# Performance work log

Hardware: AMD Instinct MI355X
Metric: run time of the kernel (lower is better)

The kernel has to match this reference:

```python
import jax, jax.numpy as jnp
import numpy as np

THRESHOLD = 0.5
NEGPOS_RATIO = 3
VARIANCES = (0.1, 0.2)

B, P, C, T = 64, 24564, 81, 50


def point_form(boxes):
    # center form (cx,cy,w,h) -> corner form (x1,y1,x2,y2)
    return jnp.concatenate([boxes[:, :2] - boxes[:, 2:] / 2,
                            boxes[:, :2] + boxes[:, 2:] / 2], axis=-1)


def jaccard(box_a, box_b):
    # box_a [T,4], box_b [P,4], corner form -> IoU [T,P]
    max_xy = jnp.minimum(box_a[:, None, 2:], box_b[None, :, 2:])
    min_xy = jnp.maximum(box_a[:, None, :2], box_b[None, :, :2])
    inter = jnp.prod(jnp.clip(max_xy - min_xy, 0.0), axis=-1)
    area_a = jnp.prod(box_a[:, 2:] - box_a[:, :2], axis=-1)[:, None]
    area_b = jnp.prod(box_b[:, 2:] - box_b[:, :2], axis=-1)[None, :]
    return inter / (area_a + area_b - inter)


def encode(matched, priors, variances):
    # matched [P,4] corner form, priors [P,4] center form
    g_cxcy = (matched[:, :2] + matched[:, 2:]) / 2 - priors[:, :2]
    g_cxcy = g_cxcy / (variances[0] * priors[:, 2:])
    g_wh = (matched[:, 2:] - matched[:, :2]) / priors[:, 2:]
    g_wh = jnp.log(g_wh) / variances[1]
    return jnp.concatenate([g_cxcy, g_wh], axis=-1)


def match_one(truths, labels, priors):
    # truths [T,4] corner, labels [T] int, priors [P,4] center form
    overlaps = jaccard(truths, point_form(priors))          # [T,P]
    best_prior_idx = jnp.argmax(overlaps, axis=1)           # [T] best prior per gt
    best_truth_overlap = jnp.max(overlaps, axis=0)          # [P]
    best_truth_idx = jnp.argmax(overlaps, axis=0)           # [P]
    # ensure every gt keeps its best prior
    best_truth_overlap = best_truth_overlap.at[best_prior_idx].set(2.0)
    best_truth_idx = best_truth_idx.at[best_prior_idx].set(jnp.arange(truths.shape[0]))
    matched = truths[best_truth_idx]                        # [P,4]
    conf = labels[best_truth_idx] + 1                       # background = 0
    conf = jnp.where(best_truth_overlap < THRESHOLD, 0, conf)
    loc = encode(matched, priors, VARIANCES)                # [P,4]
    return loc, conf


def setup_inputs() -> dict:
    key = jax.random.key(0)
    k1, k2, k3, k4, k5, k6, k7 = jax.random.split(key, 7)
    loc_data = jax.random.normal(k1, (B, P, 4), jnp.float32)
    conf_data = jax.random.normal(k2, (B, P, C), jnp.float32)
    # priors: center form, in-bounds
    ctr = 0.05 + 0.9 * jax.random.uniform(k3, (P, 2))
    wh = 0.05 + 0.25 * jax.random.uniform(k4, (P, 2))
    priors = jnp.concatenate([ctr, wh], axis=-1).astype(jnp.float32)
    # gt boxes: corner form with x2>x1, y2>y1
    xy1 = 0.7 * jax.random.uniform(k5, (B, T, 2))
    gwh = 0.05 + 0.25 * jax.random.uniform(k6, (B, T, 2))
    targets_boxes = jnp.concatenate([xy1, jnp.minimum(xy1 + gwh, 1.0)], axis=-1).astype(jnp.float32)
    targets_labels = jax.random.randint(k7, (B, T), 0, C - 1, jnp.int32)
    return {"loc_data": loc_data, "conf_data": conf_data, "priors": priors,
            "targets_boxes": targets_boxes, "targets_labels": targets_labels}


def reference(loc_data, conf_data, priors, targets_boxes, targets_labels):
    num, num_priors, _ = loc_data.shape
    # per-image matching, batched with vmap
    loc_t, conf_t = jax.vmap(lambda t, l: match_one(t, l, priors))(targets_boxes, targets_labels)
    pos = conf_t > 0                                         # [B,P]
    # localization: smooth-L1 over positives, sum
    diff = loc_data - loc_t
    ad = jnp.abs(diff)
    sl1 = jnp.where(ad < 1.0, 0.5 * diff * diff, ad - 0.5)
    loss_l = jnp.sum(sl1 * pos[..., None])
    # confidence: cross entropy = logsumexp - gathered logit
    logsm = jax.nn.log_softmax(conf_data, axis=-1)
    ce = -jnp.take_along_axis(logsm, conf_t[..., None], axis=-1)[..., 0]  # [B,P]
    # hard negative mining: rank losses among negatives
    loss_mine = jnp.where(pos, 0.0, ce)
    num_pos = jnp.sum(pos, axis=1)                           # [B]
    num_neg = jnp.minimum(NEGPOS_RATIO * num_pos, num_priors - 1)
    idx_rank = jnp.argsort(jnp.argsort(-loss_mine, axis=1), axis=1)
    neg = idx_rank < num_neg[:, None]
    loss_c = jnp.sum(jnp.where(pos | neg, ce, 0.0))
    n = jnp.maximum(jnp.sum(num_pos), 1).astype(loc_data.dtype)
    return jnp.stack([loss_l / n, loss_c / n])
```

## Files before the change

kernel.cpp:

```cpp
#include <hip/hip_runtime.h>
#include <cstdint>
#include <cstddef>

#define NB 64
#define NP 24564
#define NC 81
#define NT 50
#define NROWS (NB*NP)
#define TCH 10
#define NSEG 8
#define SEGLEN ((NP + NSEG - 1)/NSEG)

__device__ __forceinline__ unsigned long long umax64(unsigned long long a, unsigned long long b){
  return a > b ? a : b;
}

__global__ __launch_bounds__(256) void k_match(
    const float* __restrict__ priors, const float* __restrict__ tboxes,
    float* __restrict__ bto, int* __restrict__ bti)
{
  __shared__ float tb[NT*4];
  __shared__ float ta[NT];
  const int tid = threadIdx.x;
  const int b = blockIdx.y;
  if (tid < NT*4) tb[tid] = tboxes[b*NT*4 + tid];
  __syncthreads();
  if (tid < NT) ta[tid] = (tb[tid*4+2]-tb[tid*4+0]) * (tb[tid*4+3]-tb[tid*4+1]);
  __syncthreads();
  const int p = blockIdx.x*256 + tid;
  if (p >= NP) return;
  const float4 pr = ((const float4* __restrict__)priors)[p];
  const float px1 = pr.x - 0.5f*pr.z, py1 = pr.y - 0.5f*pr.w;
  const float px2 = pr.x + 0.5f*pr.z, py2 = pr.y + 0.5f*pr.w;
  const float pa  = pr.z * pr.w;
  float best = -1.0f; int bidx = 0;
  for (int t = 0; t < NT; ++t){
    const float x1 = tb[t*4+0], y1 = tb[t*4+1], x2 = tb[t*4+2], y2 = tb[t*4+3];
    float ix = fminf(x2, px2) - fmaxf(x1, px1);
    float iy = fminf(y2, py2) - fmaxf(y1, py1);
    ix = fmaxf(ix, 0.0f); iy = fmaxf(iy, 0.0f);
    const float inter = ix * iy;
    const float iou = inter / (ta[t] + pa - inter);
    if (iou > best){ best = iou; bidx = t; }
  }
  bto[b*NP + p] = best;
  bti[b*NP + p] = bidx;
}

__global__ __launch_bounds__(256) void k_bestprior(
    const float* __restrict__ priors, const float* __restrict__ tboxes,
    unsigned long long* __restrict__ bpk)
{
  __shared__ float tb[TCH*4];
  __shared__ float ta[TCH];
  __shared__ unsigned long long red[256*TCH];
  const int tid = threadIdx.x;
  const int b  = blockIdx.x;
  const int t0 = blockIdx.y * TCH;
  const int i0 = blockIdx.z * SEGLEN;
  const int iend = min(i0 + SEGLEN, NP);
  if (tid < TCH*4) tb[tid] = tboxes[(b*NT + t0)*4 + tid];
  __syncthreads();
  if (tid < TCH) ta[tid] = (tb[tid*4+2]-tb[tid*4+0]) * (tb[tid*4+3]-tb[tid*4+1]);
  __syncthreads();

  unsigned long long best[TCH];
  #pragma unroll
  for (int j = 0; j < TCH; ++j) best[j] = 0ULL;

  for (int i = i0 + tid; i < iend; i += 256){
    const float4 pr = ((const float4* __restrict__)priors)[i];
    const float px1 = pr.x - 0.5f*pr.z, py1 = pr.y - 0.5f*pr.w;
    const float px2 = pr.x + 0.5f*pr.z, py2 = pr.y + 0.5f*pr.w;
    const float pa  = pr.z * pr.w;
    const unsigned long long low = (unsigned long long)(~(unsigned)i);
    #pragma unroll
    for (int j = 0; j < TCH; ++j){
      float ix = fminf(tb[j*4+2], px2) - fmaxf(tb[j*4+0], px1);
      float iy = fminf(tb[j*4+3], py2) - fmaxf(tb[j*4+1], py1);
      ix = fmaxf(ix, 0.0f); iy = fmaxf(iy, 0.0f);
      const float inter = ix * iy;
      const float iou = inter / (ta[j] + pa - inter);
      const unsigned long long key =
          ((unsigned long long)__float_as_uint(iou) << 32) | low;
      best[j] = umax64(best[j], key);
    }
  }
  #pragma unroll
  for (int j = 0; j < TCH; ++j) red[tid*TCH + j] = best[j];
  __syncthreads();
  for (int s = 128; s > 0; s >>= 1){
    if (tid < s){
      #pragma unroll
      for (int j = 0; j < TCH; ++j)
        red[tid*TCH + j] = umax64(red[tid*TCH + j], red[(tid+s)*TCH + j]);
    }
    __syncthreads();
  }
  if (tid < TCH)
    atomicMax(&bpk[b*NT + t0 + tid], red[tid]);
}

__global__ void k_force(const unsigned long long* __restrict__ bpk,
                        float* __restrict__ bto, int* __restrict__ bti)
{
  const int b = threadIdx.x;
  if (b >= NB) return;
  for (int t = 0; t < NT; ++t){
    const int p = (int)(~(unsigned)(bpk[b*NT + t] & 0xffffffffULL));
    bto[b*NP + p] = 2.0f;
    bti[b*NP + p] = t;
  }
}

__global__ __launch_bounds__(256) void k_ce(
    const float* __restrict__ conf, const float* __restrict__ loc,
    const float* __restrict__ priors, const float* __restrict__ tboxes,
    const int* __restrict__ tlabels,
    const float* __restrict__ bto, const int* __restrict__ bti,
    float* __restrict__ mine, float* __restrict__ ce_pos,
    float* __restrict__ loss_l, int* __restrict__ num_pos)
{
  const int tid = threadIdx.x;
  const int b = blockIdx.y;
  const int p0 = blockIdx.x*256 + tid;
  const bool active = p0 < NP;
  const int p = active ? p0 : (NP - 1);
  const int r = b*NP + p;
  const size_t e0 = (size_t)r * NC;
  const size_t a0 = e0 & ~(size_t)3;
  const int s = (int)(e0 & 3);

  const float4* __restrict__ c4 = (const float4* __restrict__)conf + (a0 >> 2);
  float4 w[21];
  #pragma unroll
  for (int j = 0; j < 21; ++j) w[j] = c4[j];

  const float ov = bto[r];
  const int   ti = bti[r];
  const int  cls = (ov < 0.5f) ? 0 : (tlabels[b*NT + ti] + 1);
  const float lg = conf[e0 + cls];

  const float NI = -INFINITY;
  w[0].x  = (s > 0) ? NI : w[0].x;
  w[0].y  = (s > 1) ? NI : w[0].y;
  w[0].z  = (s > 2) ? NI : w[0].z;
  w[20].y = (s < 1) ? NI : w[20].y;
  w[20].z = (s < 2) ? NI : w[20].z;
  w[20].w = (s < 3) ? NI : w[20].w;

  float m = w[0].w;
  #pragma unroll
  for (int j = 0; j < 21; ++j)
    m = fmaxf(m, fmaxf(fmaxf(w[j].x, w[j].y), fmaxf(w[j].z, w[j].w)));

  float a0s = 0.f, a1s = 0.f, a2s = 0.f, a3s = 0.f;
  #pragma unroll
  for (int j = 0; j < 21; ++j){
    a0s += __expf(w[j].x - m);
    a1s += __expf(w[j].y - m);
    a2s += __expf(w[j].z - m);
    a3s += __expf(w[j].w - m);
  }
  const float ce = m + __logf((a0s + a1s) + (a2s + a3s)) - lg;

  const bool pos = active && (cls > 0);
  if (active) mine[r] = pos ? 0.0f : ce;

  float cp = pos ? ce : 0.0f;
  float ll = 0.0f;
  int   pc = pos ? 1 : 0;
  if (pos){
    const float4 pr = ((const float4* __restrict__)priors)[p];
    const float4 t4 = ((const float4* __restrict__)tboxes)[b*NT + ti];
    const float gcx = ((t4.x + t4.z)*0.5f - pr.x) / (0.1f*pr.z);
    const float gcy = ((t4.y + t4.w)*0.5f - pr.y) / (0.1f*pr.w);
    const float gw  = __logf((t4.z - t4.x) / pr.z) * 5.0f;
    const float gh  = __logf((t4.w - t4.y) / pr.w) * 5.0f;
    const float4 ld = ((const float4* __restrict__)loc)[r];
    float d, ad;
    d = ld.x - gcx; ad = fabsf(d); ll += (ad < 1.0f) ? 0.5f*d*d : ad - 0.5f;
    d = ld.y - gcy; ad = fabsf(d); ll += (ad < 1.0f) ? 0.5f*d*d : ad - 0.5f;
    d = ld.z - gw;  ad = fabsf(d); ll += (ad < 1.0f) ? 0.5f*d*d : ad - 0.5f;
    d = ld.w - gh;  ad = fabsf(d); ll += (ad < 1.0f) ? 0.5f*d*d : ad - 0.5f;
  }

  #pragma unroll
  for (int off = 32; off > 0; off >>= 1){
    cp += __shfl_down(cp, off);
    ll += __shfl_down(ll, off);
    pc += __shfl_down(pc, off);
  }
  __shared__ float rcp[4], rll[4];
  __shared__ int rpc[4];
  const int wv = tid >> 6;
  if ((tid & 63) == 0){ rcp[wv] = cp; rll[wv] = ll; rpc[wv] = pc; }
  __syncthreads();
  if (tid == 0){
    atomicAdd(&ce_pos[b], (rcp[0]+rcp[1])+(rcp[2]+rcp[3]));
    atomicAdd(&loss_l[b], (rll[0]+rll[1])+(rll[2]+rll[3]));
    atomicAdd(&num_pos[b], (rpc[0]+rpc[1])+(rpc[2]+rpc[3]));
  }
}

__global__ __launch_bounds__(256) void k_topk(
    const float* __restrict__ mine, const int* __restrict__ num_pos,
    float* __restrict__ topk)
{
  const int b = blockIdx.x;
  const int tid = threadIdx.x;
  const float* __restrict__ d = mine + (size_t)b * NP;
  const int k = min(3 * num_pos[b], NP - 1);

  __shared__ unsigned hist[256];
  __shared__ unsigned sfx[257];
  __shared__ unsigned s_prefix;
  __shared__ int s_rem;
  __shared__ float s_sum;

  if (k <= 0){
    if (tid == 0) topk[b] = 0.0f;
    return;
  }
  if (tid == 0){ s_prefix = 0u; s_rem = k; s_sum = 0.0f; }
  __syncthreads();

  for (int pass = 0; pass < 4; ++pass){
    const int shift = 24 - pass*8;
    hist[tid] = 0u;
    __syncthreads();
    const unsigned pref = s_prefix;
    #pragma unroll 4
    for (int i = tid; i < NP; i += 256){
      const unsigned u = __float_as_uint(d[i]);
      const bool cand = (pass == 0) || ((u >> (shift + 8)) == pref);
      if (cand) atomicAdd(&hist[(u >> shift) & 255u], 1u);
    }
    __syncthreads();
    sfx[tid] = hist[tid];
    if (tid == 0) sfx[256] = 0u;
    __syncthreads();
    for (int off = 1; off < 256; off <<= 1){
      const unsigned add = (tid + off < 256) ? sfx[tid + off] : 0u;
      __syncthreads();
      sfx[tid] += add;
      __syncthreads();
    }
    const int rem = s_rem;
    __syncthreads();
    if ((int)sfx[tid] >= rem && (int)sfx[tid + 1] < rem){
      s_prefix = (pref << 8) | (unsigned)tid;
      s_rem = rem - (int)sfx[tid + 1];
    }
    __syncthreads();
  }

  const unsigned kb = s_prefix;
  const int rem = s_rem;
  const float kv = __uint_as_float(kb);
  float acc = 0.0f;
  #pragma unroll 4
  for (int i = tid; i < NP; i += 256){
    const float x = d[i];
    if (__float_as_uint(x) > kb) acc += x;
  }
  atomicAdd(&s_sum, acc);
  __syncthreads();
  if (tid == 0) topk[b] = s_sum + (float)rem * kv;
}

__global__ void k_final(const int* __restrict__ num_pos,
                        const float* __restrict__ loss_l,
                        const float* __restrict__ ce_pos,
                        const float* __restrict__ topk,
                        float* __restrict__ out)
{
  const int tid = threadIdx.x;
  int   np = num_pos[tid];
  float ll = loss_l[tid];
  float cp = ce_pos[tid];
  float tk = topk[tid];
  #pragma unroll
  for (int off = 32; off > 0; off >>= 1){
    np += __shfl_down(np, off);
    ll += __shfl_down(ll, off);
    cp += __shfl_down(cp, off);
    tk += __shfl_down(tk, off);
  }
  if (tid == 0){
    const float n = (float)max(np, 1);
    out[0] = ll / n;
    out[1] = (cp + tk) / n;
  }
}

extern "C" void kernel_launch(void* const* d_in, const int* in_sizes, int n_in,
                              void* d_out, int out_size, void* d_ws, size_t ws_size,
                              hipStream_t stream)
{
  const float* loc     = (const float*)d_in[0];
  const float* conf    = (const float*)d_in[1];
  const float* priors  = (const float*)d_in[2];
  const float* tboxes  = (const float*)d_in[3];
  const int*   tlabels = (const int*)d_in[4];
  float* out = (float*)d_out;

  char* ws = (char*)d_ws;
  int*   num_pos = (int*)(ws + 0);
  float* loss_l  = (float*)(ws + 256);
  float* ce_pos  = (float*)(ws + 512);
  float* topk    = (float*)(ws + 768);
  unsigned long long* bpk = (unsigned long long*)(ws + 1024);
  float* bto  = (float*)(ws + 26624);
  int*   bti  = (int*)  (ws + 26624 + 4*(size_t)NROWS);
  float* mine = (float*)(ws + 26624 + 8*(size_t)NROWS);

  hipMemsetAsync(ws, 0, 26624, stream);

  dim3 gA((NP + 255)/256, NB);
  k_match<<<gA, 256, 0, stream>>>(priors, tboxes, bto, bti);

  dim3 gA2(NB, NT/TCH, NSEG);
  k_bestprior<<<gA2, 256, 0, stream>>>(priors, tboxes, bpk);

  k_force<<<1, 64, 0, stream>>>(bpk, bto, bti);

  dim3 gC((NP + 255)/256, NB);
  k_ce<<<gC, 256, 0, stream>>>(conf, loc, priors, tboxes, tlabels,
                               bto, bti, mine, ce_pos, loss_l, num_pos);

  k_topk<<<NB, 256, 0, stream>>>(mine, num_pos, topk);

  k_final<<<1, 64, 0, stream>>>(num_pos, loss_l, ce_pos, topk, out);
}
```

Before: 880.5 us.

## Fuse IoU matching into CE kernel and widen top-k selection

Removes the separate per-prior matching kernel and the force kernel. Each CE thread now computes its best-truth IoU against shared-memory truth boxes and applies the forced best-prior overrides from the packed keys, which avoids writing and re-reading the per-row overlap and index arrays. The best-prior reduction switches to wave shuffles, and its segment count goes from 8 to 16. The top-k radix select moves to 1024 threads with float4 loads and a wave-level suffix scan. The trade-off is more ALU work and shared-memory traffic inside the bandwidth-bound CE kernel.

Result: faster. 781.5 us (-11.2%).

```diff
diff --git a/kernel.cpp b/kernel.cpp
--- a/kernel.cpp
+++ b/kernel.cpp
@@ -5,46 +5,14 @@
 #define NB 64
 #define NP 24564
 #define NC 81
+#define NROWS (NB*NP)
 #define NT 50
-#define NROWS (NB*NP)
 #define TCH 10
-#define NSEG 8
-#define SEGLEN ((NP + NSEG - 1)/NSEG)
+#define NSEG 16
+#define SEGLEN 1536
 
 __device__ __forceinline__ unsigned long long umax64(unsigned long long a, unsigned long long b){
   return a > b ? a : b;
-}
-
-__global__ __launch_bounds__(256) void k_match(
-    const float* __restrict__ priors, const float* __restrict__ tboxes,
-    float* __restrict__ bto, int* __restrict__ bti)
-{
-  __shared__ float tb[NT*4];
-  __shared__ float ta[NT];
-  const int tid = threadIdx.x;
-  const int b = blockIdx.y;
-  if (tid < NT*4) tb[tid] = tboxes[b*NT*4 + tid];
-  __syncthreads();
-  if (tid < NT) ta[tid] = (tb[tid*4+2]-tb[tid*4+0]) * (tb[tid*4+3]-tb[tid*4+1]);
-  __syncthreads();
-  const int p = blockIdx.x*256 + tid;
-  if (p >= NP) return;
-  const float4 pr = ((const float4* __restrict__)priors)[p];
-  const float px1 = pr.x - 0.5f*pr.z, py1 = pr.y - 0.5f*pr.w;
-  const float px2 = pr.x + 0.5f*pr.z, py2 = pr.y + 0.5f*pr.w;
-  const float pa  = pr.z * pr.w;
-  float best = -1.0f; int bidx = 0;
-  for (int t = 0; t < NT; ++t){
-    const float x1 = tb[t*4+0], y1 = tb[t*4+1], x2 = tb[t*4+2], y2 = tb[t*4+3];
-    float ix = fminf(x2, px2) - fmaxf(x1, px1);
-    float iy = fminf(y2, py2) - fmaxf(y1, py1);
-    ix = fmaxf(ix, 0.0f); iy = fmaxf(iy, 0.0f);
-    const float inter = ix * iy;
-    const float iou = inter / (ta[t] + pa - inter);
-    if (iou > best){ best = iou; bidx = t; }
-  }
-  bto[b*NP + p] = best;
-  bti[b*NP + p] = bidx;
 }
 
 __global__ __launch_bounds__(256) void k_bestprior(
@@ -53,7 +21,7 @@
 {
   __shared__ float tb[TCH*4];
   __shared__ float ta[TCH];
-  __shared__ unsigned long long red[256*TCH];
+  __shared__ unsigned long long part[4][TCH];
   const int tid = threadIdx.x;
   const int b  = blockIdx.x;
   const int t0 = blockIdx.y * TCH;
@@ -87,29 +55,22 @@
     }
   }
   #pragma unroll
-  for (int j = 0; j < TCH; ++j) red[tid*TCH + j] = best[j];
-  __syncthreads();
-  for (int s = 128; s > 0; s >>= 1){
-    if (tid < s){
-      #pragma unroll
-      for (int j = 0; j < TCH; ++j)
-        red[tid*TCH + j] = umax64(red[tid*TCH + j], red[(tid+s)*TCH + j]);
-    }
-    __syncthreads();
-  }
-  if (tid < TCH)
-    atomicMax(&bpk[b*NT + t0 + tid], red[tid]);
-}
-
-__global__ void k_force(const unsigned long long* __restrict__ bpk,
-                        float* __restrict__ bto, int* __restrict__ bti)
-{
-  const int b = threadIdx.x;
-  if (b >= NB) return;
-  for (int t = 0; t < NT; ++t){
-    const int p = (int)(~(unsigned)(bpk[b*NT + t] & 0xffffffffULL));
-    bto[b*NP + p] = 2.0f;
-    bti[b*NP + p] = t;
+  for (int off = 32; off > 0; off >>= 1){
+    #pragma unroll
+    for (int j = 0; j < TCH; ++j)
+      best[j] = umax64(best[j], __shfl_down(best[j], off));
+  }
+  const int wv = tid >> 6;
+  if ((tid & 63) == 0){
+    #pragma unroll
+    for (int j = 0; j < TCH; ++j) part[wv][j] = best[j];
+  }
+  __syncthreads();
+  if (tid < TCH){
+    const unsigned long long m =
+        umax64(umax64(part[0][tid], part[1][tid]),
+               umax64(part[2][tid], part[3][tid]));
+    atomicMax(&bpk[b*NT + t0 + tid], m);
   }
 }
 
@@ -117,12 +78,28 @@
     const float* __restrict__ conf, const float* __restrict__ loc,
     const float* __restrict__ priors, const float* __restrict__ tboxes,
     const int* __restrict__ tlabels,
-    const float* __restrict__ bto, const int* __restrict__ bti,
+    const unsigned long long* __restrict__ bpk,
     float* __restrict__ mine, float* __restrict__ ce_pos,
     float* __restrict__ loss_l, int* __restrict__ num_pos)
 {
+  __shared__ float tb[NT*4];
+  __shared__ float ta[NT];
+  __shared__ int ips[NT];
+  __shared__ int tl[NT];
   const int tid = threadIdx.x;
   const int b = blockIdx.y;
+  if (tid < NT*4) tb[tid] = tboxes[b*NT*4 + tid];
+  else if (tid < NT*4 + NT){
+    const int t = tid - NT*4;
+    ips[t] = (int)(~(unsigned)(bpk[b*NT + t] & 0xffffffffULL));
+  }
+  __syncthreads();
+  if (tid < NT){
+    ta[tid] = (tb[tid*4+2]-tb[tid*4+0]) * (tb[tid*4+3]-tb[tid*4+1]);
+    tl[tid] = tlabels[b*NT + tid];
+  }
+  __syncthreads();
+
   const int p0 = blockIdx.x*256 + tid;
   const bool active = p0 < NP;
   const int p = active ? p0 : (NP - 1);
@@ -136,12 +113,36 @@
   #pragma unroll
   for (int j = 0; j < 21; ++j) w[j] = c4[j];
 
-  const float ov = bto[r];
-  const int   ti = bti[r];
-  const int  cls = (ov < 0.5f) ? 0 : (tlabels[b*NT + ti] + 1);
-  const float lg = conf[e0 + cls];
+  const float4 pr = ((const float4* __restrict__)priors)[p];
+  const float px1 = pr.x - 0.5f*pr.z, py1 = pr.y - 0.5f*pr.w;
+  const float px2 = pr.x + 0.5f*pr.z, py2 = pr.y + 0.5f*pr.w;
+  const float pa  = pr.z * pr.w;
+  float ov = -1.0f; int ti = 0;
+  for (int t = 0; t < NT; ++t){
+    float ix = fminf(tb[t*4+2], px2) - fmaxf(tb[t*4+0], px1);
+    float iy = fminf(tb[t*4+3], py2) - fmaxf(tb[t*4+1], py1);
+    ix = fmaxf(ix, 0.0f); iy = fmaxf(iy, 0.0f);
+    const float inter = ix * iy;
+    const float iou = inter / (ta[t] + pa - inter);
+    if (iou > ov){ ov = iou; ti = t; }
+  }
+  #pragma unroll 10
+  for (int t = 0; t < NT; ++t){
+    if (ips[t] == p){ ov = 2.0f; ti = t; }
+  }
+  const int cls = (ov < 0.5f) ? 0 : (tl[ti] + 1);
 
   const float NI = -INFINITY;
+  const int idx = s + cls;
+  float lg = 0.0f;
+  #pragma unroll
+  for (int j = 0; j < 21; ++j){
+    if ((idx >> 2) == j){
+      const float4 t4 = w[j];
+      const int q = idx & 3;
+      lg = (q == 0) ? t4.x : (q == 1) ? t4.y : (q == 2) ? t4.z : t4.w;
+    }
+  }
   w[0].x  = (s > 0) ? NI : w[0].x;
   w[0].y  = (s > 1) ? NI : w[0].y;
   w[0].z  = (s > 2) ? NI : w[0].z;
@@ -154,15 +155,15 @@
   for (int j = 0; j < 21; ++j)
     m = fmaxf(m, fmaxf(fmaxf(w[j].x, w[j].y), fmaxf(w[j].z, w[j].w)));
 
-  float a0s = 0.f, a1s = 0.f, a2s = 0.f, a3s = 0.f;
+  float s0 = 0.f, s1 = 0.f, s2 = 0.f, s3 = 0.f;
   #pragma unroll
   for (int j = 0; j < 21; ++j){
-    a0s += __expf(w[j].x - m);
-    a1s += __expf(w[j].y - m);
-    a2s += __expf(w[j].z - m);
-    a3s += __expf(w[j].w - m);
-  }
-  const float ce = m + __logf((a0s + a1s) + (a2s + a3s)) - lg;
+    s0 += __expf(w[j].x - m);
+    s1 += __expf(w[j].y - m);
+    s2 += __expf(w[j].z - m);
+    s3 += __expf(w[j].w - m);
+  }
+  const float ce = m + __logf((s0 + s1) + (s2 + s3)) - lg;
 
   const bool pos = active && (cls > 0);
   if (active) mine[r] = pos ? 0.0f : ce;
@@ -171,12 +172,11 @@
   float ll = 0.0f;
   int   pc = pos ? 1 : 0;
   if (pos){
-    const float4 pr = ((const float4* __restrict__)priors)[p];
-    const float4 t4 = ((const float4* __restrict__)tboxes)[b*NT + ti];
-    const float gcx = ((t4.x + t4.z)*0.5f - pr.x) / (0.1f*pr.z);
-    const float gcy = ((t4.y + t4.w)*0.5f - pr.y) / (0.1f*pr.w);
-    const float gw  = __logf((t4.z - t4.x) / pr.z) * 5.0f;
-    const float gh  = __logf((t4.w - t4.y) / pr.w) * 5.0f;
+    const float tx1 = tb[ti*4+0], ty1 = tb[ti*4+1], tx2 = tb[ti*4+2], ty2 = tb[ti*4+3];
+    const float gcx = ((tx1 + tx2)*0.5f - pr.x) / (0.1f*pr.z);
+    const float gcy = ((ty1 + ty2)*0.5f - pr.y) / (0.1f*pr.w);
+    const float gw  = __logf((tx2 - tx1) / pr.z) * 5.0f;
+    const float gh  = __logf((ty2 - ty1) / pr.w) * 5.0f;
     const float4 ld = ((const float4* __restrict__)loc)[r];
     float d, ad;
     d = ld.x - gcx; ad = fabsf(d); ll += (ad < 1.0f) ? 0.5f*d*d : ad - 0.5f;
@@ -203,54 +203,65 @@
   }
 }
 
-__global__ __launch_bounds__(256) void k_topk(
+__global__ __launch_bounds__(1024) void k_topk(
     const float* __restrict__ mine, const int* __restrict__ num_pos,
     float* __restrict__ topk)
 {
   const int b = blockIdx.x;
   const int tid = threadIdx.x;
-  const float* __restrict__ d = mine + (size_t)b * NP;
+  const float4* __restrict__ d4 =
+      (const float4* __restrict__)(mine + (size_t)b * NP);
   const int k = min(3 * num_pos[b], NP - 1);
 
   __shared__ unsigned hist[256];
-  __shared__ unsigned sfx[257];
   __shared__ unsigned s_prefix;
   __shared__ int s_rem;
-  __shared__ float s_sum;
+  __shared__ float wsum[16];
 
   if (k <= 0){
     if (tid == 0) topk[b] = 0.0f;
     return;
   }
-  if (tid == 0){ s_prefix = 0u; s_rem = k; s_sum = 0.0f; }
-  __syncthreads();
+  if (tid == 0){ s_prefix = 0u; s_rem = k; }
 
   for (int pass = 0; pass < 4; ++pass){
     const int shift = 24 - pass*8;
-    hist[tid] = 0u;
+    if (tid < 256) hist[tid] = 0u;
     __syncthreads();
     const unsigned pref = s_prefix;
-    #pragma unroll 4
-    for (int i = tid; i < NP; i += 256){
-      const unsigned u = __float_as_uint(d[i]);
-      const bool cand = (pass == 0) || ((u >> (shift + 8)) == pref);
-      if (cand) atomicAdd(&hist[(u >> shift) & 255u], 1u);
+    const int rem = s_rem;
+    for (int i = tid; i < 6141; i += 1024){
+      const float4 v = d4[i];
+      unsigned u;
+      u = __float_as_uint(v.x);
+      if (pass == 0 || (u >> (shift+8)) == pref) atomicAdd(&hist[(u>>shift)&255u], 1u);
+      u = __float_as_uint(v.y);
+      if (pass == 0 || (u >> (shift+8)) == pref) atomicAdd(&hist[(u>>shift)&255u], 1u);
+      u = __float_as_uint(v.z);
+      if (pass == 0 || (u >> (shift+8)) == pref) atomicAdd(&hist[(u>>shift)&255u], 1u);
+      u = __float_as_uint(v.w);
+      if (pass == 0 || (u >> (shift+8)) == pref) atomicAdd(&hist[(u>>shift)&255u], 1u);
     }
     __syncthreads();
-    sfx[tid] = hist[tid];
-    if (tid == 0) sfx[256] = 0u;
-    __syncthreads();
-    for (int off = 1; off < 256; off <<= 1){
-      const unsigned add = (tid + off < 256) ? sfx[tid + off] : 0u;
-      __syncthreads();
-      sfx[tid] += add;
-      __syncthreads();
-    }
-    const int rem = s_rem;
-    __syncthreads();
-    if ((int)sfx[tid] >= rem && (int)sfx[tid + 1] < rem){
-      s_prefix = (pref << 8) | (unsigned)tid;
-      s_rem = rem - (int)sfx[tid + 1];
+    if (tid < 64){
+      const unsigned h0 = hist[4*tid], h1 = hist[4*tid+1];
+      const unsigned h2 = hist[4*tid+2], h3 = hist[4*tid+3];
+      const unsigned pl = h0 + h1 + h2 + h3;
+      unsigned S = pl;
+      #pragma unroll
+      for (int off = 1; off < 64; off <<= 1){
+        const unsigned v = __shfl_down(S, off);
+        if (tid + off < 64) S += v;
+      }
+      const unsigned Sn = S - pl;
+      const unsigned t3 = h3 + Sn;
+      const unsigned t2 = h2 + t3;
+      const unsigned t1 = h1 + t2;
+      const unsigned t0 = h0 + t1;
+      if ((int)t0 >= rem && (int)t1 < rem){ s_prefix = (pref<<8) | (4u*tid+0u); s_rem = rem - (int)t1; }
+      if ((int)t1 >= rem && (int)t2 < rem){ s_prefix = (pref<<8) | (4u*tid+1u); s_rem = rem - (int)t2; }
+      if ((int)t2 >= rem && (int)t3 < rem){ s_prefix = (pref<<8) | (4u*tid+2u); s_rem = rem - (int)t3; }
+      if ((int)t3 >= rem && (int)Sn < rem){ s_prefix = (pref<<8) | (4u*tid+3u); s_rem = rem - (int)Sn; }
     }
     __syncthreads();
   }
@@ -259,14 +270,23 @@
   const int rem = s_rem;
   const float kv = __uint_as_float(kb);
   float acc = 0.0f;
-  #pragma unroll 4
-  for (int i = tid; i < NP; i += 256){
-    const float x = d[i];
-    if (__float_as_uint(x) > kb) acc += x;
-  }
-  atomicAdd(&s_sum, acc);
-  __syncthreads();
-  if (tid == 0) topk[b] = s_sum + (float)rem * kv;
+  for (int i = tid; i < 6141; i += 1024){
+    const float4 v = d4[i];
+    if (__float_as_uint(v.x) > kb) acc += v.x;
+    if (__float_as_uint(v.y) > kb) acc += v.y;
+    if (__float_as_uint(v.z) > kb) acc += v.z;
+    if (__float_as_uint(v.w) > kb) acc += v.w;
+  }
+  #pragma unroll
+  for (int off = 32; off > 0; off >>= 1) acc += __shfl_down(acc, off);
+  if ((tid & 63) == 0) wsum[tid >> 6] = acc;
+  __syncthreads();
+  if (tid == 0){
+    float s = 0.0f;
+    #pragma unroll
+    for (int j = 0; j < 16; ++j) s += wsum[j];
+    topk[b] = s + (float)rem * kv;
+  }
 }
 
 __global__ void k_final(const int* __restrict__ num_pos,
@@ -311,25 +331,18 @@
   float* ce_pos  = (float*)(ws + 512);
   float* topk    = (float*)(ws + 768);
   unsigned long long* bpk = (unsigned long long*)(ws + 1024);
-  float* bto  = (float*)(ws + 26624);
-  int*   bti  = (int*)  (ws + 26624 + 4*(size_t)NROWS);
-  float* mine = (float*)(ws + 26624 + 8*(size_t)NROWS);
+  float* mine = (float*)(ws + 26624);
 
   hipMemsetAsync(ws, 0, 26624, stream);
 
-  dim3 gA((NP + 255)/256, NB);
-  k_match<<<gA, 256, 0, stream>>>(priors, tboxes, bto, bti);
-
-  dim3 gA2(NB, NT/TCH, NSEG);
-  k_bestprior<<<gA2, 256, 0, stream>>>(priors, tboxes, bpk);
-
-  k_force<<<1, 64, 0, stream>>>(bpk, bto, bti);
+  dim3 gA(NB, NT/TCH, NSEG);
+  k_bestprior<<<gA, 256, 0, stream>>>(priors, tboxes, bpk);
 
   dim3 gC((NP + 255)/256, NB);
   k_ce<<<gC, 256, 0, stream>>>(conf, loc, priors, tboxes, tlabels,
-                               bto, bti, mine, ce_pos, loss_l, num_pos);
-
-  k_topk<<<NB, 256, 0, stream>>>(mine, num_pos, topk);
+                               bpk, mine, ce_pos, loss_l, num_pos);
+
+  k_topk<<<NB, 1024, 0, stream>>>(mine, num_pos, topk);
 
   k_final<<<1, 64, 0, stream>>>(num_pos, loss_l, ce_pos, topk, out);
 }
```
